# Kernel tuning notes

Hardware: AMD Instinct MI355X
Metric: run time of the kernel (lower is better)

## Reference

```python
import jax, jax.numpy as jnp
import numpy as np

H = 128; B = 2
NG = 20000; NP = 3000
E_GG = 200000; E_TG = 200000; E_GP = 200000; E_PP = 100000
TAU_TG = 0.5; TOPK_TG = 16; TAU_GP = 0.5; TOPK_GP = 32
SQRT_H = float(np.sqrt(H))


def _mlp(x, w1, b1, w2, b2):
    # build_mlp(H, [H], H): Linear -> ReLU -> Linear (dropout=0)
    return jax.nn.relu(x @ w1 + b1) @ w2 + b2


def _scatter_sum(msgs, dst, num):
    # msgs: [B, E, H] -> [B, num, H]
    b, _, h = msgs.shape
    return jnp.zeros((b, num, h), msgs.dtype).at[:, dst, :].add(msgs)


def _prune(scores, dst, topk, tau):
    # per-target top-k + threshold pruning; scores [B, E], dst [E]
    E = scores.shape[1]
    pos = jnp.arange(E)
    def one(s):
        order = jnp.lexsort((-s, dst))  # primary: dst asc, secondary: score desc
        d_sorted = dst[order]
        is_start = jnp.concatenate([jnp.ones((1,), bool), d_sorted[1:] != d_sorted[:-1]])
        seg_start = jax.lax.associative_scan(jnp.maximum, jnp.where(is_start, pos, 0))
        rank = pos - seg_start  # rank within segment (0 = largest score)
        keep_sorted = (rank < topk) & (s[order] > tau)
        keep = jnp.zeros((E,), bool).at[order].set(keep_sorted)
        return jnp.where(keep, s, 0.0)
    return jax.vmap(one)(scores)


def _forward(gene_states, pathway_states, gg_w, tg_w, gp_w, pp_w,
             mlp_gg_w1, mlp_gg_b1, mlp_gg_w2, mlp_gg_b2,
             mlp_gp_w1, mlp_gp_b1, mlp_gp_w2, mlp_gp_b2,
             mlp_pp_w1, mlp_pp_b1, mlp_pp_w2, mlp_pp_b2,
             mlp_pg_w1, mlp_pg_b1, mlp_pg_w2, mlp_pg_b2,
             w_gg, w_pp, w_pg,
             tg_q, tg_k, tg_v_tf, tg_v_gene,
             gp_q, gp_k, gp_v,
             gg_src, gg_dst, tg_src, tg_dst, gp_src, gp_dst, pp_src, pp_dst):
    # Layer 1: gene-gene message passing with fixed edge weights
    gg_msgs = (gene_states[:, gg_src, :] @ w_gg) * gg_w[None, :, None]
    h1 = _mlp(gene_states, mlp_gg_w1, mlp_gg_b1, mlp_gg_w2, mlp_gg_b2) + _scatter_sum(gg_msgs, gg_dst, NG)

    # Layer 2: TF->gene attention with per-target pruning
    q_gene = h1 @ tg_q; k_tf = h1 @ tg_k; v_tf = h1 @ tg_v_tf; v_gene = h1 @ tg_v_gene
    raw_tg = jnp.einsum('beh,beh->be', q_gene[:, tg_dst, :], k_tf[:, tg_src, :]) / SQRT_H
    tg_scores = jax.nn.sigmoid(raw_tg * tg_w[None, :])
    tg_sel = _prune(tg_scores, tg_dst, TOPK_TG, TAU_TG)
    h2 = v_gene + _scatter_sum(tg_sel[..., None] * v_tf[:, tg_src, :], tg_dst, NG)

    # Layer 3: gene->pathway attention with pruning
    q_p = pathway_states @ gp_q; k_g = h2 @ gp_k; v_g = h2 @ gp_v
    raw_gp = jnp.einsum('beh,beh->be', q_p[:, gp_dst, :], k_g[:, gp_src, :]) / SQRT_H
    gp_scores = jax.nn.sigmoid(raw_gp * gp_w[None, :])
    gp_sel = _prune(gp_scores, gp_dst, TOPK_GP, TAU_GP)
    bar_h3 = _mlp(pathway_states, mlp_gp_w1, mlp_gp_b1, mlp_gp_w2, mlp_gp_b2) + _scatter_sum(gp_sel[..., None] * v_g[:, gp_src, :], gp_dst, NP)

    # Layer 4: pathway-pathway message passing
    pp_msgs = (bar_h3[:, pp_src, :] @ w_pp) * pp_w[None, :, None]
    h3 = _mlp(bar_h3, mlp_pp_w1, mlp_pp_b1, mlp_pp_w2, mlp_pp_b2) + _scatter_sum(pp_msgs, pp_dst, NP)

    # Layer 5: pathway->gene feedback (reversed gp edges, same gp weights)
    pg_msgs = (h3[:, gp_dst, :] @ w_pg) * gp_w[None, :, None]
    final_gene = _mlp(h2, mlp_pg_w1, mlp_pg_b1, mlp_pg_w2, mlp_pg_b2) + _scatter_sum(pg_msgs, gp_src, NG)
    return final_gene, h3


def setup_inputs() -> dict:
    key = jax.random.key(0)
    ks = iter(jax.random.split(key, 64))
    W = lambda: jax.random.normal(next(ks), (H, H), jnp.float32) * 0.05
    Bv = lambda: jnp.zeros((H,), jnp.float32)
    ew = lambda n: jax.random.uniform(next(ks), (n,), jnp.float32)
    ei = lambda n, hi: jax.random.randint(next(ks), (n,), 0, hi)
    inp = {
        'gene_states': jax.random.normal(next(ks), (B, NG, H), jnp.float32),
        'pathway_states': jax.random.normal(next(ks), (B, NP, H), jnp.float32),
        'gg_w': ew(E_GG), 'tg_w': ew(E_TG), 'gp_w': ew(E_GP), 'pp_w': ew(E_PP),
        'gg_src': ei(E_GG, NG), 'gg_dst': ei(E_GG, NG),
        'tg_src': ei(E_TG, NG), 'tg_dst': ei(E_TG, NG),
        'gp_src': ei(E_GP, NG), 'gp_dst': ei(E_GP, NP),
        'pp_src': ei(E_PP, NP), 'pp_dst': ei(E_PP, NP),
    }
    for name in ['mlp_gg', 'mlp_gp', 'mlp_pp', 'mlp_pg']:
        inp[name + '_w1'] = W(); inp[name + '_b1'] = Bv()
        inp[name + '_w2'] = W(); inp[name + '_b2'] = Bv()
    for name in ['w_gg', 'w_pp', 'w_pg', 'tg_q', 'tg_k', 'tg_v_tf', 'tg_v_gene', 'gp_q', 'gp_k', 'gp_v']:
        inp[name] = W()
    return inp


def reference(gene_states, pathway_states, gg_w, tg_w, gp_w, pp_w,
              gg_src, gg_dst, tg_src, tg_dst, gp_src, gp_dst, pp_src, pp_dst,
              mlp_gg_w1, mlp_gg_b1, mlp_gg_w2, mlp_gg_b2,
              mlp_gp_w1, mlp_gp_b1, mlp_gp_w2, mlp_gp_b2,
              mlp_pp_w1, mlp_pp_b1, mlp_pp_w2, mlp_pp_b2,
              mlp_pg_w1, mlp_pg_b1, mlp_pg_w2, mlp_pg_b2,
              w_gg, w_pp, w_pg, tg_q, tg_k, tg_v_tf, tg_v_gene, gp_q, gp_k, gp_v):
    return _forward(gene_states, pathway_states, gg_w, tg_w, gp_w, pp_w,
                    mlp_gg_w1, mlp_gg_b1, mlp_gg_w2, mlp_gg_b2,
                    mlp_gp_w1, mlp_gp_b1, mlp_gp_w2, mlp_gp_b2,
                    mlp_pp_w1, mlp_pp_b1, mlp_pp_w2, mlp_pp_b2,
                    mlp_pg_w1, mlp_pg_b1, mlp_pg_w2, mlp_pg_b2,
                    w_gg, w_pp, w_pg, tg_q, tg_k, tg_v_tf, tg_v_gene, gp_q, gp_k, gp_v,
                    gg_src, gg_dst, tg_src, tg_dst, gp_src, gp_dst, pp_src, pp_dst)
```

## Files before the change

### kernel.cpp

```cpp
#include <hip/hip_runtime.h>
#include <math.h>

#define H_ 128
static constexpr int NG_ = 20000, NP_ = 3000, B_ = 2;
static constexpr int EGG_ = 200000, ETG_ = 200000, EGP_ = 200000, EPP_ = 100000;
static constexpr float TAU_ = 0.5f;
static constexpr float RSQRTH_ = 0.088388347648318447f;

struct CsrDesc {
  const int* dst;
  int E, N;
  int* cnt;
  int* cur;
  int* off;
  int* bkt;
};
struct CsrPack { CsrDesc c[5]; };

__global__ void hist_all_k(CsrPack p) {
  CsrDesc d = p.c[blockIdx.y];
  int i = blockIdx.x * 256 + threadIdx.x;
  if (i < d.E) atomicAdd(&d.cnt[d.dst[i]], 1);
}

__global__ void scatter_all_k(CsrPack p) {
  CsrDesc d = p.c[blockIdx.y];
  int i = blockIdx.x * 256 + threadIdx.x;
  if (i < d.E) {
    int t = d.dst[i];
    int pos = atomicAdd(&d.cur[t], 1);
    d.bkt[d.off[t] + pos] = i;
  }
}

__global__ void exscan_all_k(CsrPack p) {
  CsrDesc d = p.c[blockIdx.x];
  const int n = d.N;
  const int* cnt = d.cnt;
  int* off = d.off;
  __shared__ int sh[256];
  const int tid = threadIdx.x;
  if (tid == 0) off[0] = 0;
  int run = 0;
  for (int base = 0; base < n; base += 4096) {
    int loc[16];
    int s = 0;
#pragma unroll
    for (int j = 0; j < 16; ++j) {
      int i = base + tid * 16 + j;
      loc[j] = (i < n) ? cnt[i] : 0;
      s += loc[j];
    }
    sh[tid] = s;
    __syncthreads();
    for (int st = 1; st < 256; st <<= 1) {
      int v = (tid >= st) ? sh[tid - st] : 0;
      __syncthreads();
      sh[tid] += v;
      __syncthreads();
    }
    int acc = run + ((tid > 0) ? sh[tid - 1] : 0);
    int tot = sh[255];
    __syncthreads();
#pragma unroll
    for (int j = 0; j < 16; ++j) {
      int i = base + tid * 16 + j;
      acc += loc[j];
      if (i < n) off[i + 1] = acc;
    }
    run += tot;
  }
}

static constexpr int GF_RELU = 1, GF_TOLDS = 2;
struct GOp { const float* W; const float* bias; float* Y; int flags; };
struct GPack { GOp o[4]; };

template <int NOPS, int ROWS, int THREADS>
__global__ __launch_bounds__(THREADS) void gemmN_k(const float* __restrict__ X, GPack p, int R) {
  constexpr int NTY = THREADS / 32;
  constexpr int RPR = ROWS / NTY;
  __shared__ float Xl[ROWS][132];
  const int t = threadIdx.x;
  const int tx = t & 31, ty = t >> 5;
  const int r0 = blockIdx.x * ROWS;
#pragma unroll
  for (int it = 0; it < ROWS * 32 / THREADS; ++it) {
    int idx = t + THREADS * it;
    int row = idx >> 5;
    int kq = idx & 31;
    int gr = r0 + row;
    float4 v = make_float4(0.f, 0.f, 0.f, 0.f);
    if (gr < R) v = *(const float4*)&X[(size_t)gr * 128 + kq * 4];
    *(float4*)&Xl[row][kq * 4] = v;
  }
  __syncthreads();
#pragma unroll
  for (int op = 0; op < NOPS; ++op) {
    const float4* __restrict__ Wv = (const float4*)p.o[op].W;
    float acc[RPR][4];
#pragma unroll
    for (int i = 0; i < RPR; ++i)
#pragma unroll
      for (int j = 0; j < 4; ++j) acc[i][j] = 0.f;
    float4 wc[4];
#pragma unroll
    for (int j = 0; j < 4; ++j) wc[j] = Wv[j * 32 + tx];
#pragma unroll 2
    for (int k = 0; k < 128; k += 4) {
      float4 wn[4];
      const int kn = (k + 4 < 128) ? (k + 4) : 0;
#pragma unroll
      for (int j = 0; j < 4; ++j) wn[j] = Wv[(kn + j) * 32 + tx];
#pragma unroll
      for (int i = 0; i < RPR; ++i) {
        float4 xv = *(const float4*)&Xl[ty * RPR + i][k];
        acc[i][0] += xv.x * wc[0].x + xv.y * wc[1].x + xv.z * wc[2].x + xv.w * wc[3].x;
        acc[i][1] += xv.x * wc[0].y + xv.y * wc[1].y + xv.z * wc[2].y + xv.w * wc[3].y;
        acc[i][2] += xv.x * wc[0].z + xv.y * wc[1].z + xv.z * wc[2].z + xv.w * wc[3].z;
        acc[i][3] += xv.x * wc[0].w + xv.y * wc[1].w + xv.z * wc[2].w + xv.w * wc[3].w;
      }
#pragma unroll
      for (int j = 0; j < 4; ++j) wc[j] = wn[j];
    }
    float4 bv = make_float4(0.f, 0.f, 0.f, 0.f);
    if (p.o[op].bias) bv = *(const float4*)&p.o[op].bias[tx * 4];
    const bool relu = (p.o[op].flags & GF_RELU) != 0;
    if (p.o[op].flags & GF_TOLDS) {
      __syncthreads();
#pragma unroll
      for (int i = 0; i < RPR; ++i) {
        float4 o;
        o.x = acc[i][0] + bv.x; o.y = acc[i][1] + bv.y;
        o.z = acc[i][2] + bv.z; o.w = acc[i][3] + bv.w;
        if (relu) {
          o.x = fmaxf(o.x, 0.f); o.y = fmaxf(o.y, 0.f);
          o.z = fmaxf(o.z, 0.f); o.w = fmaxf(o.w, 0.f);
        }
        *(float4*)&Xl[ty * RPR + i][tx * 4] = o;
      }
      __syncthreads();
    } else {
      float* __restrict__ Y = p.o[op].Y;
#pragma unroll
      for (int i = 0; i < RPR; ++i) {
        int gr = r0 + ty * RPR + i;
        if (gr < R) {
          float4 o;
          o.x = acc[i][0] + bv.x; o.y = acc[i][1] + bv.y;
          o.z = acc[i][2] + bv.z; o.w = acc[i][3] + bv.w;
          if (relu) {
            o.x = fmaxf(o.x, 0.f); o.y = fmaxf(o.y, 0.f);
            o.z = fmaxf(o.z, 0.f); o.w = fmaxf(o.w, 0.f);
          }
          *(float4*)&Y[(size_t)gr * 128 + tx * 4] = o;
        }
      }
    }
  }
}

template <int CAP>
__global__ __launch_bounds__(256) void attn_agg_k(
    const int* __restrict__ off, const int* __restrict__ bkt,
    const int* __restrict__ fidx, const float* __restrict__ ew,
    const float* __restrict__ Q, const float* __restrict__ K,
    const float* __restrict__ V, float* __restrict__ out,
    int nT, int nS, int topk) {
  __shared__ float s_sh[4][CAP];
  __shared__ int f_sh[4][CAP];
  __shared__ int e_sh[4][CAP];
  __shared__ int c_sh[4][CAP];
  __shared__ float q_sh[4][128];
  const int wv = threadIdx.x >> 6, lane = threadIdx.x & 63;
  const int t = blockIdx.x * 4 + wv, b = blockIdx.y;
  if (t >= nT) return;
  const int o0 = off[t];
  const int ne = min(off[t + 1] - o0, CAP);
  if (ne == 0) return;

  for (int i = lane; i < ne; i += 64) {
    int e = bkt[o0 + i];
    f_sh[wv][i] = fidx[e];
    e_sh[wv][i] = e;
    s_sh[wv][i] = ew[e];
  }
  *(float2*)&q_sh[wv][lane * 2] = *(const float2*)&Q[((size_t)b * nT + t) * 128 + lane * 2];

  const int g = lane >> 3, l = lane & 7;
  float4 q[4];
#pragma unroll
  for (int j = 0; j < 4; ++j) q[j] = *(const float4*)&q_sh[wv][(l + 8 * j) * 4];
  for (int i0 = 0; i0 < ne; i0 += 8) {
    int idx = i0 + g;
    bool val = idx < ne;
    int f = f_sh[wv][val ? idx : 0];
    const float4* kr = (const float4*)&K[((size_t)b * nS + f) * 128];
    float p = 0.f;
#pragma unroll
    for (int j = 0; j < 4; ++j) {
      float4 kv = kr[l + 8 * j];
      p += kv.x * q[j].x + kv.y * q[j].y + kv.z * q[j].z + kv.w * q[j].w;
    }
    p += __shfl_xor(p, 1);
    p += __shfl_xor(p, 2);
    p += __shfl_xor(p, 4);
    if (l == 0 && val) {
      float w = s_sh[wv][idx];
      s_sh[wv][idx] = 1.f / (1.f + expf(-p * RSQRTH_ * w));
    }
  }

  float keep[(CAP + 63) / 64];
#pragma unroll
  for (int c = 0; c * 64 < CAP; ++c) {
    int i = lane + c * 64;
    float r = 0.f;
    if (i < ne) {
      float si = s_sh[wv][i];
      int ei = e_sh[wv][i];
      int cnt = 0;
      for (int j = 0; j < ne; ++j) {
        float sj = s_sh[wv][j];
        cnt += (sj > si) || (sj == si && e_sh[wv][j] < ei);
      }
      r = (cnt < topk && si > TAU_) ? si : 0.f;
    }
    keep[c] = r;
  }
#pragma unroll
  for (int c = 0; c * 64 < CAP; ++c) {
    int i = lane + c * 64;
    if (i < ne) s_sh[wv][i] = keep[c];
  }

  int nsel = 0;
  for (int c = 0; c * 64 < ne; ++c) {
    int i = c * 64 + lane;
    bool sel = (i < ne) && (s_sh[wv][i] != 0.f);
    unsigned long long m = __ballot(sel);
    int pos = __popcll(m & ((1ull << lane) - 1ull));
    if (sel) c_sh[wv][nsel + pos] = i;
    nsel += __popcll(m);
  }

  size_t orow = ((size_t)b * nT + t) * 128 + lane * 2;
  float2 acc = *(float2*)&out[orow];
  int j = 0;
  for (; j + 2 <= nsel; j += 2) {
    int i0 = c_sh[wv][j], i1 = c_sh[wv][j + 1];
    float w0 = s_sh[wv][i0], w1 = s_sh[wv][i1];
    float2 v0 = *(const float2*)&V[((size_t)b * nS + f_sh[wv][i0]) * 128 + lane * 2];
    float2 v1 = *(const float2*)&V[((size_t)b * nS + f_sh[wv][i1]) * 128 + lane * 2];
    acc.x += w0 * v0.x + w1 * v1.x;
    acc.y += w0 * v0.y + w1 * v1.y;
  }
  if (j < nsel) {
    int i0 = c_sh[wv][j];
    float w0 = s_sh[wv][i0];
    float2 v0 = *(const float2*)&V[((size_t)b * nS + f_sh[wv][i0]) * 128 + lane * 2];
    acc.x += w0 * v0.x;
    acc.y += w0 * v0.y;
  }
  *(float2*)&out[orow] = acc;
}

template <int CAP>
__global__ __launch_bounds__(256) void wagg_k(
    const int* __restrict__ off, const int* __restrict__ bkt,
    const int* __restrict__ fidx, const float* __restrict__ ew,
    const float* __restrict__ V, float* __restrict__ out, int nT, int nS) {
  __shared__ float s_sh[4][CAP];
  __shared__ int f_sh[4][CAP];
  const int wv = threadIdx.x >> 6, lane = threadIdx.x & 63;
  const int t = blockIdx.x * 4 + wv, b = blockIdx.y;
  if (t >= nT) return;
  const int o0 = off[t];
  const int ne = min(off[t + 1] - o0, CAP);
  if (ne == 0) return;
  for (int i = lane; i < ne; i += 64) {
    int e = bkt[o0 + i];
    f_sh[wv][i] = fidx[e];
    s_sh[wv][i] = ew[e];
  }
  size_t orow = ((size_t)b * nT + t) * 128 + lane * 2;
  float2 acc = *(float2*)&out[orow];
  int i = 0;
  for (; i + 2 <= ne; i += 2) {
    float w0 = s_sh[wv][i], w1 = s_sh[wv][i + 1];
    float2 v0 = *(const float2*)&V[((size_t)b * nS + f_sh[wv][i]) * 128 + lane * 2];
    float2 v1 = *(const float2*)&V[((size_t)b * nS + f_sh[wv][i + 1]) * 128 + lane * 2];
    acc.x += w0 * v0.x + w1 * v1.x;
    acc.y += w0 * v0.y + w1 * v1.y;
  }
  if (i < ne) {
    float w0 = s_sh[wv][i];
    float2 v0 = *(const float2*)&V[((size_t)b * nS + f_sh[wv][i]) * 128 + lane * 2];
    acc.x += w0 * v0.x;
    acc.y += w0 * v0.y;
  }
  *(float2*)&out[orow] = acc;
}

extern "C" void kernel_launch(void* const* d_in, const int* in_sizes, int n_in, void* d_out,
                              int out_size, void* d_ws, size_t ws_size, hipStream_t stream) {
  const float* gene = (const float*)d_in[0];
  const float* path = (const float*)d_in[1];
  const float* gg_w = (const float*)d_in[2];
  const float* tg_w = (const float*)d_in[3];
  const float* gp_w = (const float*)d_in[4];
  const float* pp_w = (const float*)d_in[5];
  const int* gg_src = (const int*)d_in[6];
  const int* gg_dst = (const int*)d_in[7];
  const int* tg_src = (const int*)d_in[8];
  const int* tg_dst = (const int*)d_in[9];
  const int* gp_src = (const int*)d_in[10];
  const int* gp_dst = (const int*)d_in[11];
  const int* pp_src = (const int*)d_in[12];
  const int* pp_dst = (const int*)d_in[13];
  const float* mgg_w1 = (const float*)d_in[14];
  const float* mgg_b1 = (const float*)d_in[15];
  const float* mgg_w2 = (const float*)d_in[16];
  const float* mgg_b2 = (const float*)d_in[17];
  const float* mgp_w1 = (const float*)d_in[18];
  const float* mgp_b1 = (const float*)d_in[19];
  const float* mgp_w2 = (const float*)d_in[20];
  const float* mgp_b2 = (const float*)d_in[21];
  const float* mpp_w1 = (const float*)d_in[22];
  const float* mpp_b1 = (const float*)d_in[23];
  const float* mpp_w2 = (const float*)d_in[24];
  const float* mpp_b2 = (const float*)d_in[25];
  const float* mpg_w1 = (const float*)d_in[26];
  const float* mpg_b1 = (const float*)d_in[27];
  const float* mpg_w2 = (const float*)d_in[28];
  const float* mpg_b2 = (const float*)d_in[29];
  const float* w_gg = (const float*)d_in[30];
  const float* w_pp = (const float*)d_in[31];
  const float* w_pg = (const float*)d_in[32];
  const float* tg_q = (const float*)d_in[33];
  const float* tg_k = (const float*)d_in[34];
  const float* tg_v_tf = (const float*)d_in[35];
  const float* tg_v_gene = (const float*)d_in[36];
  const float* gp_q = (const float*)d_in[37];
  const float* gp_k = (const float*)d_in[38];
  const float* gp_v = (const float*)d_in[39];

  float* out_final = (float*)d_out;
  float* out_h3 = (float*)d_out + (size_t)B_ * NG_ * H_;

  const size_t BNGH = (size_t)B_ * NG_ * H_;
  const size_t BNPH = (size_t)B_ * NP_ * H_;

  char* wp = (char*)d_ws;
  auto alloc = [&](size_t bytes) {
    void* p = (void*)wp;
    wp += (bytes + 255) & ~(size_t)255;
    return p;
  };
  float* G0 = (float*)alloc(BNGH * 4);
  float* G2 = (float*)alloc(BNGH * 4);
  float* G3 = (float*)alloc(BNGH * 4);
  float* G4 = (float*)alloc(BNGH * 4);
  float* G5 = (float*)alloc(BNGH * 4);
  float* P0 = (float*)alloc(BNPH * 4);
  float* P2 = (float*)alloc(BNPH * 4);
  const int NCNT = 3 * NG_ + 2 * NP_;
  int* cntbuf = (int*)alloc((size_t)NCNT * 2 * 4);
  int* cnt_gg = cntbuf;
  int* cnt_tg = cnt_gg + NG_;
  int* cnt_gps = cnt_tg + NG_;
  int* cnt_gpd = cnt_gps + NG_;
  int* cnt_pp = cnt_gpd + NP_;
  int* cur0 = cntbuf + NCNT;
  int* cur_gg = cur0;
  int* cur_tg = cur_gg + NG_;
  int* cur_gps = cur_tg + NG_;
  int* cur_gpd = cur_gps + NG_;
  int* cur_pp = cur_gpd + NP_;
  int* off_gg = (int*)alloc((size_t)(NG_ + 1) * 4);
  int* off_tg = (int*)alloc((size_t)(NG_ + 1) * 4);
  int* off_gps = (int*)alloc((size_t)(NG_ + 1) * 4);
  int* off_gpd = (int*)alloc((size_t)(NP_ + 1) * 4);
  int* off_pp = (int*)alloc((size_t)(NP_ + 1) * 4);
  int* bkt_gg = (int*)alloc((size_t)EGG_ * 4);
  int* bkt_tg = (int*)alloc((size_t)ETG_ * 4);
  int* bkt_gps = (int*)alloc((size_t)EGP_ * 4);
  int* bkt_gpd = (int*)alloc((size_t)EGP_ * 4);
  int* bkt_pp = (int*)alloc((size_t)EPP_ * 4);

  hipMemsetAsync(cntbuf, 0, (size_t)NCNT * 2 * 4, stream);
  CsrPack pk;
  pk.c[0] = {gg_dst, EGG_, NG_, cnt_gg, cur_gg, off_gg, bkt_gg};
  pk.c[1] = {tg_dst, ETG_, NG_, cnt_tg, cur_tg, off_tg, bkt_tg};
  pk.c[2] = {gp_src, EGP_, NG_, cnt_gps, cur_gps, off_gps, bkt_gps};
  pk.c[3] = {gp_dst, EGP_, NP_, cnt_gpd, cur_gpd, off_gpd, bkt_gpd};
  pk.c[4] = {pp_dst, EPP_, NP_, cnt_pp, cur_pp, off_pp, bkt_pp};
  hist_all_k<<<dim3((EGG_ + 255) / 256, 5), dim3(256), 0, stream>>>(pk);
  exscan_all_k<<<dim3(5), dim3(256), 0, stream>>>(pk);
  scatter_all_k<<<dim3((EGG_ + 255) / 256, 5), dim3(256), 0, stream>>>(pk);

  const int RG = B_ * NG_;
  const int RP = B_ * NP_;
  const dim3 gG((RG + 63) / 64), gP((RP + 15) / 16);
  const dim3 blkG(512), blkP(256), blk(256);

  {
    GPack p{};
    p.o[0] = {w_gg, nullptr, G2, 0};
    p.o[1] = {mgg_w1, mgg_b1, nullptr, GF_RELU | GF_TOLDS};
    p.o[2] = {mgg_w2, mgg_b2, G0, 0};
    gemmN_k<3, 64, 512><<<gG, blkG, 0, stream>>>(gene, p, RG);
  }
  wagg_k<128><<<dim3((NG_ + 3) / 4, B_), blk, 0, stream>>>(off_gg, bkt_gg, gg_src, gg_w, G2, G0,
                                                           NG_, NG_);
  {
    GPack p{};
    p.o[0] = {tg_q, nullptr, G2, 0};
    p.o[1] = {tg_k, nullptr, G3, 0};
    p.o[2] = {tg_v_tf, nullptr, G4, 0};
    p.o[3] = {tg_v_gene, nullptr, G5, 0};
    gemmN_k<4, 64, 512><<<gG, blkG, 0, stream>>>(G0, p, RG);
  }
  attn_agg_k<128><<<dim3((NG_ + 3) / 4, B_), blk, 0, stream>>>(
      off_tg, bkt_tg, tg_src, tg_w, G2, G3, G4, G5, NG_, NG_, 16);
  {
    GPack p{};
    p.o[0] = {gp_k, nullptr, G2, 0};
    p.o[1] = {gp_v, nullptr, G3, 0};
    gemmN_k<2, 64, 512><<<gG, blkG, 0, stream>>>(G5, p, RG);
  }
  {
    GPack p{};
    p.o[0] = {gp_q, nullptr, P0, 0};
    p.o[1] = {mgp_w1, mgp_b1, nullptr, GF_RELU | GF_TOLDS};
    p.o[2] = {mgp_w2, mgp_b2, P2, 0};
    gemmN_k<3, 16, 256><<<gP, blkP, 0, stream>>>(path, p, RP);
  }
  attn_agg_k<256><<<dim3((NP_ + 3) / 4, B_), blk, 0, stream>>>(
      off_gpd, bkt_gpd, gp_src, gp_w, P0, G2, G3, P2, NP_, NG_, 32);
  {
    GPack p{};
    p.o[0] = {w_pp, nullptr, P0, 0};
    p.o[1] = {mpp_w1, mpp_b1, nullptr, GF_RELU | GF_TOLDS};
    p.o[2] = {mpp_w2, mpp_b2, out_h3, 0};
    gemmN_k<3, 16, 256><<<gP, blkP, 0, stream>>>(P2, p, RP);
  }
  wagg_k<192><<<dim3((NP_ + 3) / 4, B_), blk, 0, stream>>>(off_pp, bkt_pp, pp_src, pp_w, P0,
                                                           out_h3, NP_, NP_);
  {
    GPack p{};
    p.o[0] = {w_pg, nullptr, P0, 0};
    gemmN_k<1, 16, 256><<<gP, blkP, 0, stream>>>(out_h3, p, RP);
  }
  {
    GPack p{};
    p.o[0] = {mpg_w1, mpg_b1, nullptr, GF_RELU | GF_TOLDS};
    p.o[1] = {mpg_w2, mpg_b2, out_final, 0};
    gemmN_k<2, 64, 512><<<gG, blkG, 0, stream>>>(G5, p, RG);
  }
  wagg_k<128><<<dim3((NG_ + 3) / 4, B_), blk, 0, stream>>>(off_gps, bkt_gps, gp_dst, gp_w, P0,
                                                           out_final, NG_, NP_);
  (void)in_sizes; (void)n_in; (void)out_size; (void)ws_size;
}
```

Before: 854.5 us.

## Retile fused GEMM kernel to 8 columns per thread and merge gene-side GEMMs

The fused multi-op GEMM kernel now uses 256-thread blocks where each thread computes 8 output columns instead of 4. Each float4 row read from shared memory is therefore reused across twice as many outputs, and the weight prefetch double-buffering is dropped. Gene-side row tiles shrink from 64 to 32, and launch bounds now request 8 blocks per SM. The separate mlp_pg GEMM over G5 is folded into the gp_k/gp_v GEMM launch, so G5 is read once and one launch is saved. The risks are higher register pressure from 8 accumulators per row and the loss of weight-load latency hiding.

```diff
diff --git a/kernel.cpp b/kernel.cpp
--- a/kernel.cpp
+++ b/kernel.cpp
@@ -76,17 +76,16 @@
 struct GOp { const float* W; const float* bias; float* Y; int flags; };
 struct GPack { GOp o[4]; };
 
-template <int NOPS, int ROWS, int THREADS>
-__global__ __launch_bounds__(THREADS) void gemmN_k(const float* __restrict__ X, GPack p, int R) {
-  constexpr int NTY = THREADS / 32;
-  constexpr int RPR = ROWS / NTY;
+template <int NOPS, int ROWS>
+__global__ __launch_bounds__(256, 8) void gemmN_k(const float* __restrict__ X, GPack p, int R) {
+  constexpr int RPR = ROWS / 16;
   __shared__ float Xl[ROWS][132];
   const int t = threadIdx.x;
-  const int tx = t & 31, ty = t >> 5;
+  const int tx = t & 15, ty = t >> 4;
   const int r0 = blockIdx.x * ROWS;
 #pragma unroll
-  for (int it = 0; it < ROWS * 32 / THREADS; ++it) {
-    int idx = t + THREADS * it;
+  for (int it = 0; it < ROWS / 8; ++it) {
+    int idx = t + 256 * it;
     int row = idx >> 5;
     int kq = idx & 31;
     int gr = r0 + row;
@@ -98,46 +97,63 @@
 #pragma unroll
   for (int op = 0; op < NOPS; ++op) {
     const float4* __restrict__ Wv = (const float4*)p.o[op].W;
-    float acc[RPR][4];
+    float acc[RPR][8];
 #pragma unroll
     for (int i = 0; i < RPR; ++i)
 #pragma unroll
-      for (int j = 0; j < 4; ++j) acc[i][j] = 0.f;
-    float4 wc[4];
-#pragma unroll
-    for (int j = 0; j < 4; ++j) wc[j] = Wv[j * 32 + tx];
+      for (int c = 0; c < 8; ++c) acc[i][c] = 0.f;
 #pragma unroll 2
     for (int k = 0; k < 128; k += 4) {
-      float4 wn[4];
-      const int kn = (k + 4 < 128) ? (k + 4) : 0;
-#pragma unroll
-      for (int j = 0; j < 4; ++j) wn[j] = Wv[(kn + j) * 32 + tx];
+      float4 w[8];
+#pragma unroll
+      for (int kk = 0; kk < 4; ++kk) {
+        w[2 * kk] = Wv[(k + kk) * 32 + tx * 2];
+        w[2 * kk + 1] = Wv[(k + kk) * 32 + tx * 2 + 1];
+      }
 #pragma unroll
       for (int i = 0; i < RPR; ++i) {
         float4 xv = *(const float4*)&Xl[ty * RPR + i][k];
-        acc[i][0] += xv.x * wc[0].x + xv.y * wc[1].x + xv.z * wc[2].x + xv.w * wc[3].x;
-        acc[i][1] += xv.x * wc[0].y + xv.y * wc[1].y + xv.z * wc[2].y + xv.w * wc[3].y;
-        acc[i][2] += xv.x * wc[0].z + xv.y * wc[1].z + xv.z * wc[2].z + xv.w * wc[3].z;
-        acc[i][3] += xv.x * wc[0].w + xv.y * wc[1].w + xv.z * wc[2].w + xv.w * wc[3].w;
-      }
-#pragma unroll
-      for (int j = 0; j < 4; ++j) wc[j] = wn[j];
-    }
-    float4 bv = make_float4(0.f, 0.f, 0.f, 0.f);
-    if (p.o[op].bias) bv = *(const float4*)&p.o[op].bias[tx * 4];
+        const float xk[4] = {xv.x, xv.y, xv.z, xv.w};
+#pragma unroll
+        for (int kk = 0; kk < 4; ++kk) {
+          acc[i][0] += xk[kk] * w[2 * kk].x;
+          acc[i][1] += xk[kk] * w[2 * kk].y;
+          acc[i][2] += xk[kk] * w[2 * kk].z;
+          acc[i][3] += xk[kk] * w[2 * kk].w;
+          acc[i][4] += xk[kk] * w[2 * kk + 1].x;
+          acc[i][5] += xk[kk] * w[2 * kk + 1].y;
+          acc[i][6] += xk[kk] * w[2 * kk + 1].z;
+          acc[i][7] += xk[kk] * w[2 * kk + 1].w;
+        }
+      }
+    }
+    float4 b0 = make_float4(0.f, 0.f, 0.f, 0.f), b1 = b0;
+    if (p.o[op].bias) {
+      b0 = *(const float4*)&p.o[op].bias[tx * 8];
+      b1 = *(const float4*)&p.o[op].bias[tx * 8 + 4];
+    }
     const bool relu = (p.o[op].flags & GF_RELU) != 0;
+#pragma unroll
+    for (int i = 0; i < RPR; ++i) {
+      float o[8];
+      o[0] = acc[i][0] + b0.x; o[1] = acc[i][1] + b0.y;
+      o[2] = acc[i][2] + b0.z; o[3] = acc[i][3] + b0.w;
+      o[4] = acc[i][4] + b1.x; o[5] = acc[i][5] + b1.y;
+      o[6] = acc[i][6] + b1.z; o[7] = acc[i][7] + b1.w;
+      if (relu) {
+#pragma unroll
+        for (int c = 0; c < 8; ++c) o[c] = fmaxf(o[c], 0.f);
+      }
+#pragma unroll
+      for (int c = 0; c < 8; ++c) acc[i][c] = o[c];
+    }
     if (p.o[op].flags & GF_TOLDS) {
       __syncthreads();
 #pragma unroll
       for (int i = 0; i < RPR; ++i) {
-        float4 o;
-        o.x = acc[i][0] + bv.x; o.y = acc[i][1] + bv.y;
-        o.z = acc[i][2] + bv.z; o.w = acc[i][3] + bv.w;
-        if (relu) {
-          o.x = fmaxf(o.x, 0.f); o.y = fmaxf(o.y, 0.f);
-          o.z = fmaxf(o.z, 0.f); o.w = fmaxf(o.w, 0.f);
-        }
-        *(float4*)&Xl[ty * RPR + i][tx * 4] = o;
+        int row = ty * RPR + i;
+        *(float4*)&Xl[row][tx * 8] = make_float4(acc[i][0], acc[i][1], acc[i][2], acc[i][3]);
+        *(float4*)&Xl[row][tx * 8 + 4] = make_float4(acc[i][4], acc[i][5], acc[i][6], acc[i][7]);
       }
       __syncthreads();
     } else {
@@ -146,14 +162,10 @@
       for (int i = 0; i < RPR; ++i) {
         int gr = r0 + ty * RPR + i;
         if (gr < R) {
-          float4 o;
-          o.x = acc[i][0] + bv.x; o.y = acc[i][1] + bv.y;
-          o.z = acc[i][2] + bv.z; o.w = acc[i][3] + bv.w;
-          if (relu) {
-            o.x = fmaxf(o.x, 0.f); o.y = fmaxf(o.y, 0.f);
-            o.z = fmaxf(o.z, 0.f); o.w = fmaxf(o.w, 0.f);
-          }
-          *(float4*)&Y[(size_t)gr * 128 + tx * 4] = o;
+          *(float4*)&Y[(size_t)gr * 128 + tx * 8] =
+              make_float4(acc[i][0], acc[i][1], acc[i][2], acc[i][3]);
+          *(float4*)&Y[(size_t)gr * 128 + tx * 8 + 4] =
+              make_float4(acc[i][4], acc[i][5], acc[i][6], acc[i][7]);
         }
       }
     }
@@ -401,15 +413,14 @@
 
   const int RG = B_ * NG_;
   const int RP = B_ * NP_;
-  const dim3 gG((RG + 63) / 64), gP((RP + 15) / 16);
-  const dim3 blkG(512), blkP(256), blk(256);
+  const dim3 gG((RG + 31) / 32), gP((RP + 15) / 16), blk(256);
 
   {
     GPack p{};
     p.o[0] = {w_gg, nullptr, G2, 0};
     p.o[1] = {mgg_w1, mgg_b1, nullptr, GF_RELU | GF_TOLDS};
     p.o[2] = {mgg_w2, mgg_b2, G0, 0};
-    gemmN_k<3, 64, 512><<<gG, blkG, 0, stream>>>(gene, p, RG);
+    gemmN_k<3, 32><<<gG, blk, 0, stream>>>(gene, p, RG);
   }
   wagg_k<128><<<dim3((NG_ + 3) / 4, B_), blk, 0, stream>>>(off_gg, bkt_gg, gg_src, gg_w, G2, G0,
                                                            NG_, NG_);
@@ -419,7 +430,7 @@
     p.o[1] = {tg_k, nullptr, G3, 0};
     p.o[2] = {tg_v_tf, nullptr, G4, 0};
     p.o[3] = {tg_v_gene, nullptr, G5, 0};
-    gemmN_k<4, 64, 512><<<gG, blkG, 0, stream>>>(G0, p, RG);
+    gemmN_k<4, 32><<<gG, blk, 0, stream>>>(G0, p, RG);
   }
   attn_agg_k<128><<<dim3((NG_ + 3) / 4, B_), blk, 0, stream>>>(
       off_tg, bkt_tg, tg_src, tg_w, G2, G3, G4, G5, NG_, NG_, 16);
@@ -427,14 +438,16 @@
     GPack p{};
     p.o[0] = {gp_k, nullptr, G2, 0};
     p.o[1] = {gp_v, nullptr, G3, 0};
-    gemmN_k<2, 64, 512><<<gG, blkG, 0, stream>>>(G5, p, RG);
+    p.o[2] = {mpg_w1, mpg_b1, nullptr, GF_RELU | GF_TOLDS};
+    p.o[3] = {mpg_w2, mpg_b2, out_final, 0};
+    gemmN_k<4, 32><<<gG, blk, 0, stream>>>(G5, p, RG);
   }
   {
     GPack p{};
     p.o[0] = {gp_q, nullptr, P0, 0};
     p.o[1] = {mgp_w1, mgp_b1, nullptr, GF_RELU | GF_TOLDS};
     p.o[2] = {mgp_w2, mgp_b2, P2, 0};
-    gemmN_k<3, 16, 256><<<gP, blkP, 0, stream>>>(path, p, RP);
+    gemmN_k<3, 16><<<gP, blk, 0, stream>>>(path, p, RP);
   }
   attn_agg_k<256><<<dim3((NP_ + 3) / 4, B_), blk, 0, stream>>>(
       off_gpd, bkt_gpd, gp_src, gp_w, P0, G2, G3, P2, NP_, NG_, 32);
@@ -443,20 +456,14 @@
     p.o[0] = {w_pp, nullptr, P0, 0};
     p.o[1] = {mpp_w1, mpp_b1, nullptr, GF_RELU | GF_TOLDS};
     p.o[2] = {mpp_w2, mpp_b2, out_h3, 0};
-    gemmN_k<3, 16, 256><<<gP, blkP, 0, stream>>>(P2, p, RP);
+    gemmN_k<3, 16><<<gP, blk, 0, stream>>>(P2, p, RP);
   }
   wagg_k<192><<<dim3((NP_ + 3) / 4, B_), blk, 0, stream>>>(off_pp, bkt_pp, pp_src, pp_w, P0,
                                                            out_h3, NP_, NP_);
   {
     GPack p{};
     p.o[0] = {w_pg, nullptr, P0, 0};
-    gemmN_k<1, 16, 256><<<gP, blkP, 0, stream>>>(out_h3, p, RP);
-  }
-  {
-    GPack p{};
-    p.o[0] = {mpg_w1, mpg_b1, nullptr, GF_RELU | GF_TOLDS};
-    p.o[1] = {mpg_w2, mpg_b2, out_final, 0};
-    gemmN_k<2, 64, 512><<<gG, blkG, 0, stream>>>(G5, p, RG);
+    gemmN_k<1, 16><<<gP, blk, 0, stream>>>(out_h3, p, RP);
   }
   wagg_k<128><<<dim3((NG_ + 3) / 4, B_), blk, 0, stream>>>(off_gps, bkt_gps, gp_dst, gp_w, P0,
                                                            out_final, NG_, NP_);
```

New measurement: 1.013 ms. 1.19x slower.

## Stage weights in shared memory and split fused GEMM chains into per-op grid

Applied to the files above, without the earlier changes.

Replaces the multi-op GEMM kernel, which staged input rows in LDS and streamed weights from global memory, with a kernel that loads one full 128x128 weight matrix into LDS and streams input rows from global memory. Each op becomes a separate blockIdx.y slice, so the ops run in parallel instead of sequentially in one block. Fused MLP chains are split into two launches with intermediate buffers G1/P1, and the pg MLP is merged into the gp_k/gp_v launch. This trades extra global round-trips for the MLP hidden activations against more parallelism and register-level weight reuse, and the 64KB LDS footprint may limit occupancy.

```diff
diff --git a/kernel.cpp b/kernel.cpp
--- a/kernel.cpp
+++ b/kernel.cpp
@@ -72,90 +72,76 @@
   }
 }
 
-static constexpr int GF_RELU = 1, GF_TOLDS = 2;
-struct GOp { const float* W; const float* bias; float* Y; int flags; };
+struct GOp { const float* W; const float* bias; float* Y; int relu; };
 struct GPack { GOp o[4]; };
 
-template <int NOPS, int ROWS, int THREADS>
-__global__ __launch_bounds__(THREADS) void gemmN_k(const float* __restrict__ X, GPack p, int R) {
-  constexpr int NTY = THREADS / 32;
-  constexpr int RPR = ROWS / NTY;
-  __shared__ float Xl[ROWS][132];
+__global__ __launch_bounds__(256, 2) void gemmW_k(const float* __restrict__ X, GPack p, int R) {
+  __shared__ float Wl[128 * 128];
+  const GOp op = p.o[blockIdx.y];
   const int t = threadIdx.x;
   const int tx = t & 31, ty = t >> 5;
-  const int r0 = blockIdx.x * ROWS;
-#pragma unroll
-  for (int it = 0; it < ROWS * 32 / THREADS; ++it) {
-    int idx = t + THREADS * it;
-    int row = idx >> 5;
-    int kq = idx & 31;
-    int gr = r0 + row;
-    float4 v = make_float4(0.f, 0.f, 0.f, 0.f);
-    if (gr < R) v = *(const float4*)&X[(size_t)gr * 128 + kq * 4];
-    *(float4*)&Xl[row][kq * 4] = v;
+  {
+    const float4* __restrict__ Wv = (const float4*)op.W;
+    float4* Wlv = (float4*)Wl;
+#pragma unroll
+    for (int i = 0; i < 16; ++i) Wlv[t + 256 * i] = Wv[t + 256 * i];
   }
   __syncthreads();
-#pragma unroll
-  for (int op = 0; op < NOPS; ++op) {
-    const float4* __restrict__ Wv = (const float4*)p.o[op].W;
-    float acc[RPR][4];
-#pragma unroll
-    for (int i = 0; i < RPR; ++i)
-#pragma unroll
-      for (int j = 0; j < 4; ++j) acc[i][j] = 0.f;
-    float4 wc[4];
-#pragma unroll
-    for (int j = 0; j < 4; ++j) wc[j] = Wv[j * 32 + tx];
-#pragma unroll 2
-    for (int k = 0; k < 128; k += 4) {
-      float4 wn[4];
-      const int kn = (k + 4 < 128) ? (k + 4) : 0;
-#pragma unroll
-      for (int j = 0; j < 4; ++j) wn[j] = Wv[(kn + j) * 32 + tx];
-#pragma unroll
-      for (int i = 0; i < RPR; ++i) {
-        float4 xv = *(const float4*)&Xl[ty * RPR + i][k];
-        acc[i][0] += xv.x * wc[0].x + xv.y * wc[1].x + xv.z * wc[2].x + xv.w * wc[3].x;
-        acc[i][1] += xv.x * wc[0].y + xv.y * wc[1].y + xv.z * wc[2].y + xv.w * wc[3].y;
-        acc[i][2] += xv.x * wc[0].z + xv.y * wc[1].z + xv.z * wc[2].z + xv.w * wc[3].z;
-        acc[i][3] += xv.x * wc[0].w + xv.y * wc[1].w + xv.z * wc[2].w + xv.w * wc[3].w;
+  const int r0 = blockIdx.x * 64 + ty * 8;
+  const float* xb[8];
+#pragma unroll
+  for (int i = 0; i < 8; ++i) {
+    int gr = r0 + i;
+    if (gr >= R) gr = R - 1;
+    xb[i] = X + (size_t)gr * 128;
+  }
+  float acc[8][4];
+#pragma unroll
+  for (int i = 0; i < 8; ++i)
+#pragma unroll
+    for (int j = 0; j < 4; ++j) acc[i][j] = 0.f;
+
+  float4 wc[4], xc[8];
+#pragma unroll
+  for (int j = 0; j < 4; ++j) wc[j] = *(const float4*)&Wl[j * 128 + tx * 4];
+#pragma unroll
+  for (int i = 0; i < 8; ++i) xc[i] = *(const float4*)(xb[i]);
+
+  for (int k = 0; k < 128; k += 4) {
+    float4 wn[4], xn[8];
+    const int kn = (k + 4 < 128) ? (k + 4) : 0;
+#pragma unroll
+    for (int j = 0; j < 4; ++j) wn[j] = *(const float4*)&Wl[(kn + j) * 128 + tx * 4];
+#pragma unroll
+    for (int i = 0; i < 8; ++i) xn[i] = *(const float4*)(xb[i] + kn);
+#pragma unroll
+    for (int i = 0; i < 8; ++i) {
+      float4 xv = xc[i];
+      acc[i][0] += xv.x * wc[0].x + xv.y * wc[1].x + xv.z * wc[2].x + xv.w * wc[3].x;
+      acc[i][1] += xv.x * wc[0].y + xv.y * wc[1].y + xv.z * wc[2].y + xv.w * wc[3].y;
+      acc[i][2] += xv.x * wc[0].z + xv.y * wc[1].z + xv.z * wc[2].z + xv.w * wc[3].z;
+      acc[i][3] += xv.x * wc[0].w + xv.y * wc[1].w + xv.z * wc[2].w + xv.w * wc[3].w;
+    }
+#pragma unroll
+    for (int j = 0; j < 4; ++j) wc[j] = wn[j];
+#pragma unroll
+    for (int i = 0; i < 8; ++i) xc[i] = xn[i];
+  }
+  float4 bv = make_float4(0.f, 0.f, 0.f, 0.f);
+  if (op.bias) bv = *(const float4*)&op.bias[tx * 4];
+  float* __restrict__ Y = op.Y;
+#pragma unroll
+  for (int i = 0; i < 8; ++i) {
+    int gr = r0 + i;
+    if (gr < R) {
+      float4 o;
+      o.x = acc[i][0] + bv.x; o.y = acc[i][1] + bv.y;
+      o.z = acc[i][2] + bv.z; o.w = acc[i][3] + bv.w;
+      if (op.relu) {
+        o.x = fmaxf(o.x, 0.f); o.y = fmaxf(o.y, 0.f);
+        o.z = fmaxf(o.z, 0.f); o.w = fmaxf(o.w, 0.f);
       }
-#pragma unroll
-      for (int j = 0; j < 4; ++j) wc[j] = wn[j];
-    }
-    float4 bv = make_float4(0.f, 0.f, 0.f, 0.f);
-    if (p.o[op].bias) bv = *(const float4*)&p.o[op].bias[tx * 4];
-    const bool relu = (p.o[op].flags & GF_RELU) != 0;
-    if (p.o[op].flags & GF_TOLDS) {
-      __syncthreads();
-#pragma unroll
-      for (int i = 0; i < RPR; ++i) {
-        float4 o;
-        o.x = acc[i][0] + bv.x; o.y = acc[i][1] + bv.y;
-        o.z = acc[i][2] + bv.z; o.w = acc[i][3] + bv.w;
-        if (relu) {
-          o.x = fmaxf(o.x, 0.f); o.y = fmaxf(o.y, 0.f);
-          o.z = fmaxf(o.z, 0.f); o.w = fmaxf(o.w, 0.f);
-        }
-        *(float4*)&Xl[ty * RPR + i][tx * 4] = o;
-      }
-      __syncthreads();
-    } else {
-      float* __restrict__ Y = p.o[op].Y;
-#pragma unroll
-      for (int i = 0; i < RPR; ++i) {
-        int gr = r0 + ty * RPR + i;
-        if (gr < R) {
-          float4 o;
-          o.x = acc[i][0] + bv.x; o.y = acc[i][1] + bv.y;
-          o.z = acc[i][2] + bv.z; o.w = acc[i][3] + bv.w;
-          if (relu) {
-            o.x = fmaxf(o.x, 0.f); o.y = fmaxf(o.y, 0.f);
-            o.z = fmaxf(o.z, 0.f); o.w = fmaxf(o.w, 0.f);
-          }
-          *(float4*)&Y[(size_t)gr * 128 + tx * 4] = o;
-        }
-      }
+      *(float4*)&Y[(size_t)gr * 128 + tx * 4] = o;
     }
   }
 }
@@ -358,11 +344,13 @@
     return p;
   };
   float* G0 = (float*)alloc(BNGH * 4);
+  float* G1 = (float*)alloc(BNGH * 4);
   float* G2 = (float*)alloc(BNGH * 4);
   float* G3 = (float*)alloc(BNGH * 4);
   float* G4 = (float*)alloc(BNGH * 4);
   float* G5 = (float*)alloc(BNGH * 4);
   float* P0 = (float*)alloc(BNPH * 4);
+  float* P1 = (float*)alloc(BNPH * 4);
   float* P2 = (float*)alloc(BNPH * 4);
   const int NCNT = 3 * NG_ + 2 * NP_;
   int* cntbuf = (int*)alloc((size_t)NCNT * 2 * 4);
@@ -401,15 +389,22 @@
 
   const int RG = B_ * NG_;
   const int RP = B_ * NP_;
-  const dim3 gG((RG + 63) / 64), gP((RP + 15) / 16);
-  const dim3 blkG(512), blkP(256), blk(256);
+  const int nbG = (RG + 63) / 64, nbP = (RP + 63) / 64;
+  const dim3 blk(256);
+  auto gemm = [&](const float* X, GPack& p, int nch, int R, int nb) {
+    gemmW_k<<<dim3(nb, nch), blk, 0, stream>>>(X, p, R);
+  };
 
   {
     GPack p{};
     p.o[0] = {w_gg, nullptr, G2, 0};
-    p.o[1] = {mgg_w1, mgg_b1, nullptr, GF_RELU | GF_TOLDS};
-    p.o[2] = {mgg_w2, mgg_b2, G0, 0};
-    gemmN_k<3, 64, 512><<<gG, blkG, 0, stream>>>(gene, p, RG);
+    p.o[1] = {mgg_w1, mgg_b1, G1, 1};
+    gemm(gene, p, 2, RG, nbG);
+  }
+  {
+    GPack p{};
+    p.o[0] = {mgg_w2, mgg_b2, G0, 0};
+    gemm(G1, p, 1, RG, nbG);
   }
   wagg_k<128><<<dim3((NG_ + 3) / 4, B_), blk, 0, stream>>>(off_gg, bkt_gg, gg_src, gg_w, G2, G0,
                                                            NG_, NG_);
@@ -419,7 +414,7 @@
     p.o[1] = {tg_k, nullptr, G3, 0};
     p.o[2] = {tg_v_tf, nullptr, G4, 0};
     p.o[3] = {tg_v_gene, nullptr, G5, 0};
-    gemmN_k<4, 64, 512><<<gG, blkG, 0, stream>>>(G0, p, RG);
+    gemm(G0, p, 4, RG, nbG);
   }
   attn_agg_k<128><<<dim3((NG_ + 3) / 4, B_), blk, 0, stream>>>(
       off_tg, bkt_tg, tg_src, tg_w, G2, G3, G4, G5, NG_, NG_, 16);
@@ -427,36 +422,44 @@
     GPack p{};
     p.o[0] = {gp_k, nullptr, G2, 0};
     p.o[1] = {gp_v, nullptr, G3, 0};
-    gemmN_k<2, 64, 512><<<gG, blkG, 0, stream>>>(G5, p, RG);
+    p.o[2] = {mpg_w1, mpg_b1, G1, 1};
+    gemm(G5, p, 3, RG, nbG);
+  }
+  {
+    GPack p{};
+    p.o[0] = {mpg_w2, mpg_b2, out_final, 0};
+    gemm(G1, p, 1, RG, nbG);
   }
   {
     GPack p{};
     p.o[0] = {gp_q, nullptr, P0, 0};
-    p.o[1] = {mgp_w1, mgp_b1, nullptr, GF_RELU | GF_TOLDS};
-    p.o[2] = {mgp_w2, mgp_b2, P2, 0};
-    gemmN_k<3, 16, 256><<<gP, blkP, 0, stream>>>(path, p, RP);
+    p.o[1] = {mgp_w1, mgp_b1, P1, 1};
+    gemm(path, p, 2, RP, nbP);
+  }
+  {
+    GPack p{};
+    p.o[0] = {mgp_w2, mgp_b2, P2, 0};
+    gemm(P1, p, 1, RP, nbP);
   }
   attn_agg_k<256><<<dim3((NP_ + 3) / 4, B_), blk, 0, stream>>>(
       off_gpd, bkt_gpd, gp_src, gp_w, P0, G2, G3, P2, NP_, NG_, 32);
   {
     GPack p{};
     p.o[0] = {w_pp, nullptr, P0, 0};
-    p.o[1] = {mpp_w1, mpp_b1, nullptr, GF_RELU | GF_TOLDS};
-    p.o[2] = {mpp_w2, mpp_b2, out_h3, 0};
-    gemmN_k<3, 16, 256><<<gP, blkP, 0, stream>>>(P2, p, RP);
+    p.o[1] = {mpp_w1, mpp_b1, P1, 1};
+    gemm(P2, p, 2, RP, nbP);
+  }
+  {
+    GPack p{};
+    p.o[0] = {mpp_w2, mpp_b2, out_h3, 0};
+    gemm(P1, p, 1, RP, nbP);
   }
   wagg_k<192><<<dim3((NP_ + 3) / 4, B_), blk, 0, stream>>>(off_pp, bkt_pp, pp_src, pp_w, P0,
                                                            out_h3, NP_, NP_);
   {
     GPack p{};
     p.o[0] = {w_pg, nullptr, P0, 0};
-    gemmN_k<1, 16, 256><<<gP, blkP, 0, stream>>>(out_h3, p, RP);
-  }
-  {
-    GPack p{};
-    p.o[0] = {mpg_w1, mpg_b1, nullptr, GF_RELU | GF_TOLDS};
-    p.o[1] = {mpg_w2, mpg_b2, out_final, 0};
-    gemmN_k<2, 64, 512><<<gG, blkG, 0, stream>>>(G5, p, RG);
+    gemm(out_h3, p, 1, RP, nbP);
   }
   wagg_k<128><<<dim3((NG_ + 3) / 4, B_), blk, 0, stream>>>(off_gps, bkt_gps, gp_dst, gp_w, P0,
                                                            out_final, NG_, NP_);
```

Result: faster. 818.6 us (-4.2%).
